# Performance work log

Measured on AMD Instinct MI355X. Metric: run time of the kernel, lower is better.

Reference implementation:

```python
import jax, jax.numpy as jnp
import numpy as np

H = 32  # hidden size (hardcoded in source module)

def setup_inputs() -> dict:
    key = jax.random.key(0)
    ks = jax.random.split(key, 7)
    s = 1.0 / np.sqrt(H)  # PyTorch LSTM/Linear init scale
    return {
        "x":    jax.random.normal(ks[0], (8192, 512, 1), dtype=jnp.float32),
        "W_ih": jax.random.uniform(ks[1], (4 * H, 1), minval=-s, maxval=s, dtype=jnp.float32),
        "W_hh": jax.random.uniform(ks[2], (4 * H, H), minval=-s, maxval=s, dtype=jnp.float32),
        "b_ih": jax.random.uniform(ks[3], (4 * H,), minval=-s, maxval=s, dtype=jnp.float32),
        "b_hh": jax.random.uniform(ks[4], (4 * H,), minval=-s, maxval=s, dtype=jnp.float32),
        "W_fc": jax.random.uniform(ks[5], (1, H), minval=-s, maxval=s, dtype=jnp.float32),
        "b_fc": jax.random.uniform(ks[6], (1,), minval=-s, maxval=s, dtype=jnp.float32),
    }

def reference(x, W_ih, W_hh, b_ih, b_hh, W_fc, b_fc):
    B = x.shape[0]
    # Precompute input projections for all timesteps: [B, T, 4H]
    xg = jnp.einsum('bti,gi->btg', x, W_ih) + (b_ih + b_hh)
    xg_t = jnp.swapaxes(xg, 0, 1)  # [T, B, 4H] for scan over time

    def step(carry, xgt):
        h, c = carry
        gates = xgt + h @ W_hh.T           # [B, 4H]
        i, f, g, o = jnp.split(gates, 4, axis=-1)  # PyTorch gate order i,f,g,o
        i = jax.nn.sigmoid(i)
        f = jax.nn.sigmoid(f)
        g = jnp.tanh(g)
        o = jax.nn.sigmoid(o)
        c = f * c + i * g
        h = o * jnp.tanh(c)
        return (h, c), None

    h0 = jnp.zeros((B, H), dtype=x.dtype)
    c0 = jnp.zeros((B, H), dtype=x.dtype)
    (h_last, _), _ = jax.lax.scan(step, (h0, c0), xg_t)
    # Final linear head on last timestep hidden state: [B, output_size]
    return h_last @ W_fc.T + b_fc
```

## Files before the change

### kernel.cpp

```cpp
#include <hip/hip_runtime.h>


#define TT 512
#define HH 32
#define L2E 1.44269504088896340736f

typedef short bf16x8 __attribute__((ext_vector_type(8)));
typedef float f32x4 __attribute__((ext_vector_type(4)));

__device__ __forceinline__ short f2bf(float f) {
    unsigned u = __float_as_uint(f);
    u = (u + 0x7FFFu + ((u >> 16) & 1u)) >> 16;
    return (short)u;
}
__device__ __forceinline__ float bf2f(short s) {
    return __uint_as_float(((unsigned)(unsigned short)s) << 16);
}
__device__ __forceinline__ float fastrcp(float x) { return __builtin_amdgcn_rcpf(x); }
__device__ __forceinline__ float exp2f_(float x) { return __builtin_amdgcn_exp2f(x); }

__device__ __forceinline__ int unit_of_pos(int p) {
    return (p & 1) ? (16 + (p >> 1)) : (p >> 1);
}

#define HS   72
#define XROW 132

__launch_bounds__(512, 4)
__global__ void lstm_kernel(const float* __restrict__ x,
                            const float* __restrict__ W_ih,
                            const float* __restrict__ W_hh,
                            const float* __restrict__ b_ih,
                            const float* __restrict__ b_hh,
                            const float* __restrict__ W_fc,
                            const float* __restrict__ b_fc,
                            float* __restrict__ out) {
    __shared__ short hh0[16 * HS], hl0[16 * HS];
    __shared__ short hh1[16 * HS], hl1[16 * HS];
    __shared__ float xbuf[16 * XROW];

    const int tid  = threadIdx.x;
    const int lane = tid & 63;
    const int w    = tid >> 6;
    const int c    = lane & 15;
    const int q    = lane >> 4;
    const int k0   = q * 8;
    const int base = blockIdx.x * 16;

    const int arow = 32 * (c & 3) + 4 * w + (c >> 2);
    const float asc = ((c & 3) == 2) ? (2.0f * L2E) : (-L2E);
    bf16x8 wah, wal;
    #pragma unroll
    for (int j = 0; j < 8; ++j) {
        const float wf = W_hh[arow * HH + unit_of_pos(k0 + j)] * asc;
        const short hi = f2bf(wf);
        wah[j] = hi;
        wal[j] = f2bf(wf - bf2f(hi));
    }

    const int u = 4 * w + q;
    float wihs[4], bcs[4];
    #pragma unroll
    for (int r = 0; r < 4; ++r) {
        const float sc = (r == 2) ? (2.0f * L2E) : (-L2E);
        wihs[r] = W_ih[32 * r + u] * sc;
        bcs[r]  = (b_ih[32 * r + u] + b_hh[32 * r + u]) * sc;
    }
    const int hwoff = c * HS + 2 * (u & 15) + (u >> 4);
    const int hroff = c * HS + k0;

    for (int i = tid; i < 16 * HS; i += 512) { hh0[i] = 0; hl0[i] = 0; }

    float cs = 0.f;

    const int xrow = tid >> 5;
    const int xj4  = (tid & 31) * 4;

    __syncthreads();

    #define STEP(t, rh, rl, wh_, wl_)                                        \
    {                                                                        \
        const bf16x8 bh = *(const bf16x8*)&rh[hroff];                        \
        const bf16x8 bl = *(const bf16x8*)&rl[hroff];                        \
        const float xc = xbuf[c * XROW + ((t) & 127)];                       \
        f32x4 acc;                                                           \
        _Pragma("unroll")                                                    \
        for (int r = 0; r < 4; ++r) acc[r] = wihs[r] * xc + bcs[r];          \
        acc = __builtin_amdgcn_mfma_f32_16x16x32_bf16(wah, bh, acc, 0, 0, 0);\
        acc = __builtin_amdgcn_mfma_f32_16x16x32_bf16(wah, bl, acc, 0, 0, 0);\
        acc = __builtin_amdgcn_mfma_f32_16x16x32_bf16(wal, bh, acc, 0, 0, 0);\
        const float Ei = exp2f_(acc[0]);                                     \
        const float Ef = exp2f_(acc[1]);                                     \
        const float G  = exp2f_(acc[2]);                                     \
        const float Eo = exp2f_(acc[3]);                                     \
        const float fg  = fastrcp(1.f + Ef);                                 \
        const float igg = (G - 1.f) * fastrcp((1.f + Ei) * (G + 1.f));       \
        cs = fg * cs + igg;                                                  \
        float yc = cs * (2.0f * L2E);                                        \
        yc = fminf(60.f, fmaxf(-60.f, yc));                                  \
        const float C = exp2f_(yc);                                          \
        const float h = (C - 1.f) * fastrcp((C + 1.f) * (1.f + Eo));         \
        const short h16 = f2bf(h);                                           \
        wh_[hwoff] = h16;                                                    \
        wl_[hwoff] = f2bf(h - bf2f(h16));                                    \
        __syncthreads();                                                     \
    }

    for (int t = 0; t < TT; t += 2) {
        if ((t & 127) == 0) {
            const float4 v = *(const float4*)&x[(base + xrow) * TT + t + xj4];
            *(float4*)&xbuf[xrow * XROW + xj4] = v;
            __syncthreads();
        }
        STEP(t,     hh0, hl0, hh1, hl1);
        STEP(t + 1, hh1, hl1, hh0, hl0);
    }

    if (tid < 16) {
        float s = b_fc[0];
        #pragma unroll
        for (int p = 0; p < 32; ++p) {
            const float hv = bf2f(hh0[tid * HS + p]) + bf2f(hl0[tid * HS + p]);
            s += hv * W_fc[unit_of_pos(p)];
        }
        out[base + tid] = s;
    }
}

extern "C" void kernel_launch(void* const* d_in, const int* in_sizes, int n_in,
                              void* d_out, int out_size, void* d_ws, size_t ws_size,
                              hipStream_t stream) {
    const float* x    = (const float*)d_in[0];
    const float* W_ih = (const float*)d_in[1];
    const float* W_hh = (const float*)d_in[2];
    const float* b_ih = (const float*)d_in[3];
    const float* b_hh = (const float*)d_in[4];
    const float* W_fc = (const float*)d_in[5];
    const float* b_fc = (const float*)d_in[6];
    float* out = (float*)d_out;

    const int B = 8192;
    lstm_kernel<<<B / 16, 512, 0, stream>>>(x, W_ih, W_hh, b_ih, b_hh,
                                            W_fc, b_fc, out);
}
```

Before: 291.9 us.

## Halve block to 4 waves with two hidden units per lane and packed h stores

Each block now runs 256 threads (4 waves) instead of 8. Each lane computes two hidden units, so it holds two sets of W_hh fragments and issues six MFMAs per step instead of three. The hidden-state shared layout changes to a dense 512-element buffer per half, written with packed bf16x2 stores. The cell update is rewritten to use a single reciprocal, and the x projection is added after the MFMA rather than seeding the accumulator. The aim is cheaper per-step barriers and better latency hiding through more independent work per lane, at the cost of more registers and a longer serial chain per wave.

```diff
diff --git a/kernel.cpp b/kernel.cpp
--- a/kernel.cpp
+++ b/kernel.cpp
@@ -1,4 +1,5 @@
 #include <hip/hip_runtime.h>
+#include <hip/hip_bf16.h>
 
 
 #define TT 512
@@ -19,14 +20,9 @@
 __device__ __forceinline__ float fastrcp(float x) { return __builtin_amdgcn_rcpf(x); }
 __device__ __forceinline__ float exp2f_(float x) { return __builtin_amdgcn_exp2f(x); }
 
-__device__ __forceinline__ int unit_of_pos(int p) {
-    return (p & 1) ? (16 + (p >> 1)) : (p >> 1);
-}
-
-#define HS   72
 #define XROW 132
 
-__launch_bounds__(512, 4)
+__launch_bounds__(256, 2)
 __global__ void lstm_kernel(const float* __restrict__ x,
                             const float* __restrict__ W_ih,
                             const float* __restrict__ W_hh,
@@ -35,8 +31,8 @@
                             const float* __restrict__ W_fc,
                             const float* __restrict__ b_fc,
                             float* __restrict__ out) {
-    __shared__ short hh0[16 * HS], hl0[16 * HS];
-    __shared__ short hh1[16 * HS], hl1[16 * HS];
+    __shared__ short hhp[2][512];
+    __shared__ short hlp[2][512];
     __shared__ float xbuf[16 * XROW];
 
     const int tid  = threadIdx.x;
@@ -44,84 +40,108 @@
     const int w    = tid >> 6;
     const int c    = lane & 15;
     const int q    = lane >> 4;
-    const int k0   = q * 8;
     const int base = blockIdx.x * 16;
 
-    const int arow = 32 * (c & 3) + 4 * w + (c >> 2);
-    const float asc = ((c & 3) == 2) ? (2.0f * L2E) : (-L2E);
-    bf16x8 wah, wal;
+    const int gate = c & 3;
+    const float asc = (gate == 2) ? (2.0f * L2E) : (-L2E);
+    const int wrow0 = gate * 32 + 8 * (c >> 2);
+    bf16x8 wah[2], wal[2];
     #pragma unroll
-    for (int j = 0; j < 8; ++j) {
-        const float wf = W_hh[arow * HH + unit_of_pos(k0 + j)] * asc;
-        const short hi = f2bf(wf);
-        wah[j] = hi;
-        wal[j] = f2bf(wf - bf2f(hi));
+    for (int tt = 0; tt < 2; ++tt) {
+        const int t8 = 2 * w + tt;
+        #pragma unroll
+        for (int j = 0; j < 8; ++j) {
+            const float wf = W_hh[(wrow0 + t8) * HH + 8 * q + j] * asc;
+            const short hi = f2bf(wf);
+            wah[tt][j] = hi;
+            wal[tt][j] = f2bf(wf - bf2f(hi));
+        }
     }
 
-    const int u = 4 * w + q;
-    float wihs[4], bcs[4];
+    float wihs[2][4];
+    f32x4 bcs[2];
     #pragma unroll
-    for (int r = 0; r < 4; ++r) {
-        const float sc = (r == 2) ? (2.0f * L2E) : (-L2E);
-        wihs[r] = W_ih[32 * r + u] * sc;
-        bcs[r]  = (b_ih[32 * r + u] + b_hh[32 * r + u]) * sc;
+    for (int tt = 0; tt < 2; ++tt) {
+        const int u = 8 * q + 2 * w + tt;
+        #pragma unroll
+        for (int r = 0; r < 4; ++r) {
+            const float sc = (r == 2) ? (2.0f * L2E) : (-L2E);
+            wihs[tt][r] = W_ih[32 * r + u] * sc;
+            bcs[tt][r]  = (b_ih[32 * r + u] + b_hh[32 * r + u]) * sc;
+        }
     }
-    const int hwoff = c * HS + 2 * (u & 15) + (u >> 4);
-    const int hroff = c * HS + k0;
 
-    for (int i = tid; i < 16 * HS; i += 512) { hh0[i] = 0; hl0[i] = 0; }
+    #pragma unroll
+    for (int i = tid; i < 512; i += 256) { hhp[0][i] = 0; hlp[0][i] = 0; }
 
-    float cs = 0.f;
+    float cs[2] = {0.f, 0.f};
 
-    const int xrow = tid >> 5;
-    const int xj4  = (tid & 31) * 4;
+    const int xrow = tid >> 4;
+    const int xj4  = (tid & 15) * 4;
 
-    __syncthreads();
+    const int rdo = q * 128 + c * 8;
+    const int wro = q * 128 + c * 8 + 2 * w;
 
-    #define STEP(t, rh, rl, wh_, wl_)                                        \
-    {                                                                        \
-        const bf16x8 bh = *(const bf16x8*)&rh[hroff];                        \
-        const bf16x8 bl = *(const bf16x8*)&rl[hroff];                        \
-        const float xc = xbuf[c * XROW + ((t) & 127)];                       \
-        f32x4 acc;                                                           \
-        _Pragma("unroll")                                                    \
-        for (int r = 0; r < 4; ++r) acc[r] = wihs[r] * xc + bcs[r];          \
-        acc = __builtin_amdgcn_mfma_f32_16x16x32_bf16(wah, bh, acc, 0, 0, 0);\
-        acc = __builtin_amdgcn_mfma_f32_16x16x32_bf16(wah, bl, acc, 0, 0, 0);\
-        acc = __builtin_amdgcn_mfma_f32_16x16x32_bf16(wal, bh, acc, 0, 0, 0);\
-        const float Ei = exp2f_(acc[0]);                                     \
-        const float Ef = exp2f_(acc[1]);                                     \
-        const float G  = exp2f_(acc[2]);                                     \
-        const float Eo = exp2f_(acc[3]);                                     \
-        const float fg  = fastrcp(1.f + Ef);                                 \
-        const float igg = (G - 1.f) * fastrcp((1.f + Ei) * (G + 1.f));       \
-        cs = fg * cs + igg;                                                  \
-        float yc = cs * (2.0f * L2E);                                        \
-        yc = fminf(60.f, fmaxf(-60.f, yc));                                  \
-        const float C = exp2f_(yc);                                          \
-        const float h = (C - 1.f) * fastrcp((C + 1.f) * (1.f + Eo));         \
-        const short h16 = f2bf(h);                                           \
-        wh_[hwoff] = h16;                                                    \
-        wl_[hwoff] = f2bf(h - bf2f(h16));                                    \
-        __syncthreads();                                                     \
+    #define STEP(t, RP, WP)                                                   \
+    {                                                                         \
+        const bf16x8 bh = *(const bf16x8*)&hhp[RP][rdo];                      \
+        const bf16x8 bl = *(const bf16x8*)&hlp[RP][rdo];                      \
+        const float xc = xbuf[c * XROW + ((t) & 127)];                        \
+        f32x4 acc[2];                                                         \
+        _Pragma("unroll")                                                     \
+        for (int tt = 0; tt < 2; ++tt) {                                      \
+            f32x4 a = bcs[tt];                                                \
+            a = __builtin_amdgcn_mfma_f32_16x16x32_bf16(wah[tt], bh, a, 0,0,0);\
+            a = __builtin_amdgcn_mfma_f32_16x16x32_bf16(wah[tt], bl, a, 0,0,0);\
+            a = __builtin_amdgcn_mfma_f32_16x16x32_bf16(wal[tt], bh, a, 0,0,0);\
+            acc[tt] = a;                                                      \
+        }                                                                     \
+        float hv[2];                                                          \
+        _Pragma("unroll")                                                     \
+        for (int tt = 0; tt < 2; ++tt) {                                      \
+            const float Ei = exp2f_(acc[tt][0] + wihs[tt][0] * xc);           \
+            const float Ef = exp2f_(acc[tt][1] + wihs[tt][1] * xc);           \
+            const float G  = exp2f_(acc[tt][2] + wihs[tt][2] * xc);           \
+            const float Eo = exp2f_(acc[tt][3] + wihs[tt][3] * xc);           \
+            const float aig = (1.f + Ei) * (G + 1.f);                         \
+            const float af  = 1.f + Ef;                                       \
+            const float num = cs[tt] * aig + (G - 1.f) * af;                  \
+            const float cn  = num * fastrcp(af * aig);                        \
+            cs[tt] = cn;                                                      \
+            float yc = cn * (2.0f * L2E);                                     \
+            yc = fminf(60.f, fmaxf(-60.f, yc));                               \
+            const float C = exp2f_(yc);                                       \
+            hv[tt] = (C - 1.f) * fastrcp((C + 1.f) * (1.f + Eo));             \
+        }                                                                     \
+        union { __hip_bfloat162 b; int i; } ph, pl;                           \
+        ph.b = __float22bfloat162_rn(make_float2(hv[0], hv[1]));              \
+        const float h0h = bf2f((short)(ph.i & 0xFFFF));                       \
+        const float h1h = bf2f((short)((unsigned)ph.i >> 16));                \
+        pl.b = __float22bfloat162_rn(make_float2(hv[0] - h0h, hv[1] - h1h));  \
+        *(int*)&hhp[WP][wro] = ph.i;                                          \
+        *(int*)&hlp[WP][wro] = pl.i;                                          \
+        __syncthreads();                                                      \
     }
 
     for (int t = 0; t < TT; t += 2) {
         if ((t & 127) == 0) {
-            const float4 v = *(const float4*)&x[(base + xrow) * TT + t + xj4];
-            *(float4*)&xbuf[xrow * XROW + xj4] = v;
+            #pragma unroll
+            for (int s = 0; s < 2; ++s) {
+                const float4 v = *(const float4*)&x[(base + xrow) * TT + t + xj4 + 64 * s];
+                *(float4*)&xbuf[xrow * XROW + xj4 + 64 * s] = v;
+            }
             __syncthreads();
         }
-        STEP(t,     hh0, hl0, hh1, hl1);
-        STEP(t + 1, hh1, hl1, hh0, hl0);
+        STEP(t,     0, 1);
+        STEP(t + 1, 1, 0);
     }
 
     if (tid < 16) {
         float s = b_fc[0];
         #pragma unroll
-        for (int p = 0; p < 32; ++p) {
-            const float hv = bf2f(hh0[tid * HS + p]) + bf2f(hl0[tid * HS + p]);
-            s += hv * W_fc[unit_of_pos(p)];
+        for (int u = 0; u < 32; ++u) {
+            const int off = (u >> 3) * 128 + tid * 8 + (u & 7);
+            s += (bf2f(hhp[0][off]) + bf2f(hlp[0][off])) * W_fc[u];
         }
         out[base + tid] = s;
     }
@@ -140,6 +160,6 @@
     float* out = (float*)d_out;
 
     const int B = 8192;
-    lstm_kernel<<<B / 16, 512, 0, stream>>>(x, W_ih, W_hh, b_ih, b_hh,
+    lstm_kernel<<<B / 16, 256, 0, stream>>>(x, W_ih, W_hh, b_ih, b_hh,
                                             W_fc, b_fc, out);
 }
```

Result: faster. 282.9 us (-3.1%).
